# Performance work log

Measured on AMD Instinct MI355X. Metric: run time of the kernel, lower is better.

Reference implementation:

```python
import jax, jax.numpy as jnp
import numpy as np

N_HEAD = 8


def _forward(q, k, v, mask, gr_mask, adj, Wq, Wk, Wv, Wq2, Wk2, Wv2, Wfc,
             grW1, grb1, grW2, grb2, ln_g, ln_b):
    B, Lq, Eq, D = q.shape
    Lk, Ek = k.shape[1], k.shape[2]
    H = N_HEAD
    dk = Wq.shape[-1] // H
    dv = Wv.shape[-1] // H
    scale = dk ** 0.5
    # per-ensemble projections (i: q-ensemble, j: k-ensemble) -> [B,L,E,H,d]
    qp = jnp.einsum('blid,idf->blif', q, Wq).reshape(B, Lq, Eq, H, dk)
    qp2 = jnp.einsum('blid,idf->blif', q, Wq2).reshape(B, Lq, Eq, H, dk)
    kp = jnp.einsum('bljd,jdf->bljf', k, Wk).reshape(B, Lk, Ek, H, dk)
    kp2 = jnp.einsum('bljd,jdf->bljf', k, Wk2).reshape(B, Lk, Ek, H, dk)
    vp = jnp.einsum('bljd,jdf->bljf', v, Wv).reshape(B, Lk, Ek, H, dv)
    # (Wv2 projections are computed in the torch module but never used.)
    # scores for all (i, j, h) pairs at once: [B,Eq,H,Lq,Lk,Ek]
    s1 = jnp.einsum('bqihd,bkjhd->bihqkj', qp, kp) / scale
    s2 = jnp.einsum('bqihd,bkjhd->bihqkj', qp2, kp2) / scale
    at = jnp.tril(adj)[:, None, None, :, :, None]  # typed-edge gate
    scores = s1 * at + s2 * (1.0 - at)
    # gated graph-attention mask MLP, vectorized over (i,j,h)
    t = gr_mask.transpose(0, 2, 3, 1)  # [B,Lq,Lk,KG]
    h1 = jax.nn.relu(jnp.einsum('bqlg,ijhgm->ijhbqlm', t, grW1)
                     + grb1[:, :, :, None, None, None, :])
    agg = jnp.einsum('ijhbqlm,ijhm->ijhbql', h1, grW2) + grb2[:, :, :, None, None, None]
    agg = jnp.where(mask[None, None, None] == 1, agg, 0.0)  # zero where mask==0
    scores = scores + jnp.transpose(jax.nn.log_sigmoid(agg), (3, 0, 2, 4, 5, 1))
    scores = jnp.where(mask[:, None, None, :, :, None] == 0, -1e9, scores)
    # softmax jointly over (Lk, Ek), Ek fastest, matching the torch view
    attn = jax.nn.softmax(scores.reshape(B, Eq, H, Lq, Lk * Ek), axis=-1)
    attn = attn.reshape(B, Eq, H, Lq, Lk, Ek)
    pre = jnp.einsum('bihqke,bkehd->bqihd', attn, vp).reshape(B, Lq, Eq, H * dv)
    out = jnp.einsum('bqif,ifd->bqid', pre, Wfc) + q  # residual
    mu = out.mean(-1, keepdims=True)
    var = out.var(-1, keepdims=True)
    return (out - mu) / jnp.sqrt(var + 1e-6) * ln_g + ln_b


def setup_inputs() -> dict:
    ks = jax.random.split(jax.random.key(0), 16)
    B, L, Eq, Ek, D, KG = 4, 256, 2, 2, 512, 16
    H, dk, dv = N_HEAD, 64, 64
    s = 0.05
    return {
        'q': jax.random.normal(ks[0], (B, L, Eq, D)),
        'k': jax.random.normal(ks[1], (B, L, Ek, D)),
        'v': jax.random.normal(ks[2], (B, L, Ek, D)),
        'mask': jax.random.randint(ks[3], (B, L, L), 0, 2, dtype=jnp.int32),
        'gr_mask': jax.random.normal(ks[4], (B, KG, L, L)),
        'adj': jax.random.uniform(ks[5], (B, L, L)),
        'Wq': jax.random.normal(ks[6], (Eq, D, H * dk)) * s,
        'Wk': jax.random.normal(ks[7], (Ek, D, H * dk)) * s,
        'Wv': jax.random.normal(ks[8], (Ek, D, H * dv)) * s,
        'Wq2': jax.random.normal(ks[9], (Eq, D, H * dk)) * s,
        'Wk2': jax.random.normal(ks[10], (Ek, D, H * dk)) * s,
        'Wv2': jax.random.normal(ks[11], (Ek, D, H * dv)) * s,
        'Wfc': jax.random.normal(ks[12], (Eq, H * dv, D)) * s,
        'grW1': jax.random.normal(ks[13], (Eq, Ek, H, KG, KG)) * s,
        'grb1': jnp.zeros((Eq, Ek, H, KG)),
        'grW2': jax.random.normal(ks[14], (Eq, Ek, H, KG)) * s,
        'grb2': jnp.zeros((Eq, Ek, H)),
        'ln_g': jnp.ones((D,)),
        'ln_b': jnp.zeros((D,)),
    }


def reference(q, k, v, mask, gr_mask, adj, Wq, Wk, Wv, Wq2, Wk2, Wv2, Wfc,
              grW1, grb1, grW2, grb2, ln_g, ln_b):
    return _forward(q, k, v, mask, gr_mask, adj, Wq, Wk, Wv, Wq2, Wk2, Wv2, Wfc,
                    grW1, grb1, grW2, grb2, ln_g, ln_b)
```

## Files before the change

### kernel.cpp

```cpp
#include <hip/hip_runtime.h>


typedef short  s16x8 __attribute__((ext_vector_type(8)));
typedef float  f32x4 __attribute__((ext_vector_type(4)));

static __device__ __forceinline__ float4 ld4(const float* p) {
    return *reinterpret_cast<const float4*>(p);
}
static __device__ __forceinline__ ushort f2bf(float f) {
    unsigned u = __float_as_uint(f);
    return (ushort)((u + 0x7fffu + ((u >> 16) & 1u)) >> 16);
}
static __device__ __forceinline__ float bf2f(ushort u) {
    return __uint_as_float((unsigned)u << 16);
}

__global__ __launch_bounds__(256) void gemm_k(
    const float* __restrict__ qin, const float* __restrict__ kin, const float* __restrict__ vin,
    const float* __restrict__ Wq, const float* __restrict__ Wk, const float* __restrict__ Wv,
    const float* __restrict__ Wq2, const float* __restrict__ Wk2,
    const float* __restrict__ prebuf, const float* __restrict__ Wfc,
    ushort* __restrict__ qp, ushort* __restrict__ qp2, ushort* __restrict__ kp,
    ushort* __restrict__ kp2, ushort* __restrict__ vpT, float* __restrict__ fcb,
    int mm_base)
{
    __shared__ float As[64][17];
    __shared__ float Bs[16][64];

    const int mm = mm_base + (int)blockIdx.z;
    const float* A; const float* W; ushort* Du = nullptr; int ens; int mode;
    switch (mm) {
        case 0:  A=qin;    W=Wq;           Du=qp;   ens=0; mode=0; break;
        case 1:  A=qin;    W=Wq + 262144;  Du=qp;   ens=1; mode=0; break;
        case 2:  A=qin;    W=Wq2;          Du=qp2;  ens=0; mode=0; break;
        case 3:  A=qin;    W=Wq2 + 262144; Du=qp2;  ens=1; mode=0; break;
        case 4:  A=kin;    W=Wk;           Du=kp;   ens=0; mode=0; break;
        case 5:  A=kin;    W=Wk + 262144;  Du=kp;   ens=1; mode=0; break;
        case 6:  A=kin;    W=Wk2;          Du=kp2;  ens=0; mode=0; break;
        case 7:  A=kin;    W=Wk2 + 262144; Du=kp2;  ens=1; mode=0; break;
        case 8:  A=vin;    W=Wv;           Du=vpT;  ens=0; mode=1; break;
        case 9:  A=vin;    W=Wv + 262144;  Du=vpT;  ens=1; mode=1; break;
        case 10: A=prebuf; W=Wfc;                   ens=0; mode=2; break;
        default: A=prebuf; W=Wfc + 262144;          ens=1; mode=2; break;
    }

    const int tid = threadIdx.x;
    const int m0 = blockIdx.y * 64;
    const int n0 = blockIdx.x * 64;
    const int ty = tid >> 4, tx = tid & 15;
    const int ar = tid >> 2, ac = (tid & 3) * 4;
    const int br = tid >> 4, bc = (tid & 15) * 4;

    float acc[4][4] = {};

    for (int kt = 0; kt < 512; kt += 16) {
        float4 av = ld4(A + (size_t)(m0 + ar) * 1024 + ens * 512 + kt + ac);
        float4 bv = ld4(W + (size_t)(kt + br) * 512 + n0 + bc);
        __syncthreads();
        As[ar][ac + 0] = av.x; As[ar][ac + 1] = av.y;
        As[ar][ac + 2] = av.z; As[ar][ac + 3] = av.w;
        *reinterpret_cast<float4*>(&Bs[br][bc]) = bv;
        __syncthreads();
        #pragma unroll
        for (int kk = 0; kk < 16; ++kk) {
            float a0 = As[ty*4+0][kk];
            float a1 = As[ty*4+1][kk];
            float a2 = As[ty*4+2][kk];
            float a3 = As[ty*4+3][kk];
            float4 b4 = *reinterpret_cast<const float4*>(&Bs[kk][tx*4]);
            acc[0][0] += a0*b4.x; acc[0][1] += a0*b4.y; acc[0][2] += a0*b4.z; acc[0][3] += a0*b4.w;
            acc[1][0] += a1*b4.x; acc[1][1] += a1*b4.y; acc[1][2] += a1*b4.z; acc[1][3] += a1*b4.w;
            acc[2][0] += a2*b4.x; acc[2][1] += a2*b4.y; acc[2][2] += a2*b4.z; acc[2][3] += a2*b4.w;
            acc[3][0] += a3*b4.x; acc[3][1] += a3*b4.y; acc[3][2] += a3*b4.z; acc[3][3] += a3*b4.w;
        }
    }

    const int hh = n0 >> 6;
    if (mode == 0) {
        #pragma unroll
        for (int u = 0; u < 4; ++u) {
            const int m = m0 + ty * 4 + u;
            const int bb = m >> 8, l = m & 255;
            ushort4 o;
            o.x = f2bf(acc[u][0]); o.y = f2bf(acc[u][1]);
            o.z = f2bf(acc[u][2]); o.w = f2bf(acc[u][3]);
            *reinterpret_cast<ushort4*>(
                Du + ((size_t)((bb*2 + ens)*8 + hh) * 256 + l) * 64 + tx*4) = o;
        }
    } else if (mode == 1) {
        #pragma unroll
        for (int u = 0; u < 4; ++u) {
            const int m = m0 + ty * 4 + u;
            const int bb = m >> 8, l = m & 255;
            #pragma unroll
            for (int w = 0; w < 4; ++w) {
                const int d = tx*4 + w;
                Du[(size_t)(bb*8 + hh) * 32768 + (size_t)d * 512 + l*2 + ens] =
                    f2bf(acc[u][w]);
            }
        }
    } else {
        #pragma unroll
        for (int u = 0; u < 4; ++u) {
            const int m = m0 + ty * 4 + u;
            #pragma unroll
            for (int w = 0; w < 4; ++w)
                fcb[((size_t)m*2 + ens) * 512 + n0 + tx*4 + w] = acc[u][w];
        }
    }
}

__global__ __launch_bounds__(256) void mlp_mfma(
    const float* __restrict__ gr_mask, const int* __restrict__ mask,
    const float* __restrict__ grW1, const float* __restrict__ grb1,
    const float* __restrict__ grW2, const float* __restrict__ grb2,
    float* __restrict__ scores)
{
    __shared__ __align__(16) ushort ts[256][40];
    __shared__ __align__(16) ushort w1b[32][16][32];
    __shared__ __align__(16) float  b1s[32][16];
    __shared__ __align__(16) float  w2s[32][16];
    __shared__ float b2s[32];
    __shared__ ushort ls[256][33];

    const int tid = threadIdx.x;
    const int bq = blockIdx.x;
    const int b = bq >> 8, q = bq & 255;

    unsigned* w1w = (unsigned*)&w1b[0][0][0];
    #pragma unroll
    for (int it = 0; it < 32; ++it) w1w[tid + it*256] = 0;
    unsigned* tsw = (unsigned*)&ts[0][0];
    #pragma unroll
    for (int it = 0; it < 8; ++it) {
        int flat = tid + it*256;
        tsw[(flat >> 3) * 20 + 8 + (flat & 7)] = 0;
    }
    __syncthreads();

    #pragma unroll
    for (int g = 0; g < 16; ++g)
        ts[tid][g] = f2bf(gr_mask[(size_t)(b*16 + g) * 65536 + q*256 + tid]);
    #pragma unroll
    for (int it = 0; it < 32; ++it) {
        int flat = tid + it*256;
        int c = flat >> 8, m = (flat >> 4) & 15, g = flat & 15;
        w1b[c][m][g] = f2bf(grW1[c*256 + g*16 + m]);
    }
    #pragma unroll
    for (int it = 0; it < 2; ++it) {
        int flat = tid + it*256;
        b1s[flat >> 4][flat & 15] = grb1[flat];
        w2s[flat >> 4][flat & 15] = grW2[flat];
    }
    if (tid < 32) b2s[tid] = grb2[tid];
    __syncthreads();

    const int wv = tid >> 6, lane = tid & 63;
    const int lr = lane & 15, mg = lane >> 4;

    s16x8 tf[4];
    #pragma unroll
    for (int lt = 0; lt < 4; ++lt) {
        int l = (wv*4 + lt)*16 + lr;
        tf[lt] = *reinterpret_cast<const s16x8*>(&ts[l][mg*8]);
    }

    #pragma unroll 1
    for (int c = 0; c < 32; ++c) {
        s16x8 af  = *reinterpret_cast<const s16x8*>(&w1b[c][lr][mg*8]);
        f32x4 b1v = *reinterpret_cast<const f32x4*>(&b1s[c][mg*4]);
        f32x4 w2v = *reinterpret_cast<const f32x4*>(&w2s[c][mg*4]);
        const float b2v = b2s[c];

        f32x4 acc[4];
        #pragma unroll
        for (int lt = 0; lt < 4; ++lt)
            acc[lt] = __builtin_amdgcn_mfma_f32_16x16x32_bf16(af, tf[lt], b1v, 0, 0, 0);

        #pragma unroll
        for (int lt = 0; lt < 4; ++lt) {
            float s = fmaxf(acc[lt][0], 0.f) * w2v[0];
            s = fmaf(fmaxf(acc[lt][1], 0.f), w2v[1], s);
            s = fmaf(fmaxf(acc[lt][2], 0.f), w2v[2], s);
            s = fmaf(fmaxf(acc[lt][3], 0.f), w2v[3], s);
            s += __shfl_xor(s, 16);
            s += __shfl_xor(s, 32);
            if (lane < 16)
                ls[(wv*4 + lt)*16 + lane][c] = f2bf(s + b2v);
        }
    }
    __syncthreads();

    const int mv = mask[(size_t)(b*256 + q)*256 + tid];
    #pragma unroll 1
    for (int c2 = 0; c2 < 32; ++c2) {
        float agv = bf2f(ls[tid][c2]);
        if (mv == 0) agv = 0.f;
        float lsig = fminf(agv, 0.f) - log1pf(expf(-fabsf(agv)));
        int ii = c2 >> 4, jj = (c2 >> 3) & 1, hh = c2 & 7;
        scores[((size_t)((b*2 + ii)*8 + hh)*256 + q)*512 + (size_t)tid*2 + jj] = lsig;
    }
}

__global__ __launch_bounds__(256) void scores_mfma(
    const ushort* __restrict__ qp, const ushort* __restrict__ qp2,
    const ushort* __restrict__ kp, const ushort* __restrict__ kp2,
    const float* __restrict__ adj, const int* __restrict__ mask,
    float* __restrict__ scores)
{
    __shared__ __align__(16) ushort q1t[128*64];
    __shared__ __align__(16) ushort q2t[128*64];
    __shared__ __align__(16) ushort k1t[128*64];
    __shared__ __align__(16) ushort k2t[128*64];

    const int z = blockIdx.z;
    const int bih = z >> 1, j = z & 1;
    const int b = bih >> 4, h = bih & 7;
    const int bjh = (b*2 + j)*8 + h;
    const int q0 = blockIdx.x * 128, k0 = blockIdx.y * 128;
    const int tid = threadIdx.x;

    const ushort* gq1 = qp  + (size_t)bih * 16384 + q0 * 64;
    const ushort* gq2 = qp2 + (size_t)bih * 16384 + q0 * 64;
    const ushort* gk1 = kp  + (size_t)bjh * 16384 + k0 * 64;
    const ushort* gk2 = kp2 + (size_t)bjh * 16384 + k0 * 64;
    #pragma unroll
    for (int it = 0; it < 4; ++it) {
        int ch = tid + it * 256;
        int row = ch >> 3, c8 = ch & 7;
        int byte = row * 128 + c8 * 16; byte ^= (row & 7) << 4;
        *reinterpret_cast<uint4*>((char*)q1t + byte) = *reinterpret_cast<const uint4*>(gq1 + ch*8);
        *reinterpret_cast<uint4*>((char*)q2t + byte) = *reinterpret_cast<const uint4*>(gq2 + ch*8);
        *reinterpret_cast<uint4*>((char*)k1t + byte) = *reinterpret_cast<const uint4*>(gk1 + ch*8);
        *reinterpret_cast<uint4*>((char*)k2t + byte) = *reinterpret_cast<const uint4*>(gk2 + ch*8);
    }
    __syncthreads();

    const int wv = tid >> 6, lane = tid & 63;
    const int lr = lane & 15, kg = lane >> 4;

    #pragma unroll 1
    for (int qi = 0; qi < 2; ++qi) {
        const int qt = wv * 2 + qi;
        s16x8 a1[2], a2[2];
        #pragma unroll
        for (int ks = 0; ks < 2; ++ks) {
            int row = qt*16 + lr;
            int byte = row*128 + (ks*32 + kg*8)*2; byte ^= (row & 7) << 4;
            a1[ks] = *reinterpret_cast<const s16x8*>((const char*)q1t + byte);
            a2[ks] = *reinterpret_cast<const s16x8*>((const char*)q2t + byte);
        }
        #pragma unroll 1
        for (int kt = 0; kt < 8; ++kt) {
            f32x4 acc1 = {0.f, 0.f, 0.f, 0.f};
            f32x4 acc2 = {0.f, 0.f, 0.f, 0.f};
            #pragma unroll
            for (int ks = 0; ks < 2; ++ks) {
                int row = kt*16 + lr;
                int byte = row*128 + (ks*32 + kg*8)*2; byte ^= (row & 7) << 4;
                s16x8 b1 = *reinterpret_cast<const s16x8*>((const char*)k1t + byte);
                s16x8 b2 = *reinterpret_cast<const s16x8*>((const char*)k2t + byte);
                acc1 = __builtin_amdgcn_mfma_f32_16x16x32_bf16(a1[ks], b1, acc1, 0, 0, 0);
                acc2 = __builtin_amdgcn_mfma_f32_16x16x32_bf16(a2[ks], b2, acc2, 0, 0, 0);
            }
            const int kgl = k0 + kt*16 + lr;
            #pragma unroll
            for (int r = 0; r < 4; ++r) {
                const int qg = q0 + qt*16 + kg*4 + r;
                const size_t mi = (size_t)(b*256 + qg) * 256 + kgl;
                float gate = (qg >= kgl) ? adj[mi] : 0.f;
                float s = (acc1[r]*gate + acc2[r]*(1.f - gate)) * 0.125f;
                const size_t sidx = ((size_t)bih * 256 + qg) * 512 + (size_t)kgl * 2 + j;
                s += scores[sidx];
                if (mask[mi] == 0) s = -1e9f;
                scores[sidx] = s;
            }
        }
    }
}

__global__ __launch_bounds__(256) void softmax_k(float* __restrict__ scores,
                                                 ushort* __restrict__ attn_bf)
{
    const int row  = blockIdx.x * 4 + (threadIdx.x >> 6);
    const int lane = threadIdx.x & 63;
    float* p = scores + (size_t)row * 512 + lane * 8;
    float4 v0 = *reinterpret_cast<float4*>(p);
    float4 v1 = *reinterpret_cast<float4*>(p + 4);
    float v[8] = {v0.x, v0.y, v0.z, v0.w, v1.x, v1.y, v1.z, v1.w};

    float m = v[0];
    #pragma unroll
    for (int t = 1; t < 8; ++t) m = fmaxf(m, v[t]);
    #pragma unroll
    for (int off = 32; off > 0; off >>= 1) m = fmaxf(m, __shfl_xor(m, off));

    float s = 0.f;
    #pragma unroll
    for (int t = 0; t < 8; ++t) { v[t] = expf(v[t] - m); s += v[t]; }
    #pragma unroll
    for (int off = 32; off > 0; off >>= 1) s += __shfl_xor(s, off);

    const float inv = 1.f / s;
    #pragma unroll
    for (int t = 0; t < 8; ++t) v[t] *= inv;
    *reinterpret_cast<float4*>(p)     = make_float4(v[0], v[1], v[2], v[3]);
    *reinterpret_cast<float4*>(p + 4) = make_float4(v[4], v[5], v[6], v[7]);

    ushort* pb = attn_bf + (size_t)row * 512 + lane * 8;
    ushort4 lo, hi;
    lo.x = f2bf(v[0]); lo.y = f2bf(v[1]); lo.z = f2bf(v[2]); lo.w = f2bf(v[3]);
    hi.x = f2bf(v[4]); hi.y = f2bf(v[5]); hi.z = f2bf(v[6]); hi.w = f2bf(v[7]);
    *reinterpret_cast<ushort4*>(pb)     = lo;
    *reinterpret_cast<ushort4*>(pb + 4) = hi;
}

__global__ __launch_bounds__(256) void pv_mfma(
    const ushort* __restrict__ attn, const ushort* __restrict__ vpT,
    float* __restrict__ pre)
{
    __shared__ __align__(16) ushort at_t[64*128];
    __shared__ __align__(16) ushort v_t[64*128];

    const int bih = blockIdx.y;
    const int b = bih >> 4, i = (bih >> 3) & 1, h = bih & 7;
    const int q0 = blockIdx.x * 64;
    const int tid = threadIdx.x;
    const int wv = tid >> 6, lane = tid & 63;
    const int lr = lane & 15, kg = lane >> 4;

    const ushort* ga = attn + ((size_t)bih * 256 + q0) * 512;
    const ushort* gv = vpT + (size_t)(b*8 + h) * 32768;

    f32x4 acc[4];
    #pragma unroll
    for (int dt = 0; dt < 4; ++dt) acc[dt] = (f32x4){0.f, 0.f, 0.f, 0.f};

    #pragma unroll 1
    for (int kc = 0; kc < 4; ++kc) {
        __syncthreads();
        #pragma unroll
        for (int it = 0; it < 4; ++it) {
            int ch = tid + it * 256;
            int row = ch >> 4, c8 = ch & 15;
            int byte = row * 256 + c8 * 16; byte ^= (row & 7) << 4;
            *reinterpret_cast<uint4*>((char*)at_t + byte) =
                *reinterpret_cast<const uint4*>(ga + (size_t)row*512 + kc*128 + c8*8);
            *reinterpret_cast<uint4*>((char*)v_t + byte) =
                *reinterpret_cast<const uint4*>(gv + (size_t)row*512 + kc*128 + c8*8);
        }
        __syncthreads();
        #pragma unroll
        for (int ks = 0; ks < 4; ++ks) {
            int arow = wv*16 + lr;
            int abyte = arow*256 + (ks*32 + kg*8)*2; abyte ^= (arow & 7) << 4;
            s16x8 a = *reinterpret_cast<const s16x8*>((const char*)at_t + abyte);
            #pragma unroll
            for (int dt = 0; dt < 4; ++dt) {
                int vrow = dt*16 + lr;
                int vbyte = vrow*256 + (ks*32 + kg*8)*2; vbyte ^= (vrow & 7) << 4;
                s16x8 bv = *reinterpret_cast<const s16x8*>((const char*)v_t + vbyte);
                acc[dt] = __builtin_amdgcn_mfma_f32_16x16x32_bf16(a, bv, acc[dt], 0, 0, 0);
            }
        }
    }

    #pragma unroll
    for (int dt = 0; dt < 4; ++dt) {
        const int d = dt*16 + lr;
        #pragma unroll
        for (int r = 0; r < 4; ++r) {
            const int qg = q0 + wv*16 + kg*4 + r;
            pre[((size_t)(b*256 + qg)*2 + i) * 512 + h*64 + d] = acc[dt][r];
        }
    }
}

__global__ __launch_bounds__(256) void ln_k(
    const float* __restrict__ fcb, const float* __restrict__ qin,
    const float* __restrict__ lng, const float* __restrict__ lnb,
    float* __restrict__ out)
{
    __shared__ float red[8];
    const int row = blockIdx.x;
    const int tid = threadIdx.x;
    const float* fr = fcb + (size_t)row * 512;
    const float* qr = qin + (size_t)row * 512;
    float v0 = fr[tid]       + qr[tid];
    float v1 = fr[tid + 256] + qr[tid + 256];
    float s  = v0 + v1;
    float sq = v0*v0 + v1*v1;
    #pragma unroll
    for (int off = 32; off > 0; off >>= 1) {
        s  += __shfl_xor(s, off);
        sq += __shfl_xor(sq, off);
    }
    const int w = tid >> 6;
    if ((tid & 63) == 0) { red[w*2] = s; red[w*2 + 1] = sq; }
    __syncthreads();
    s  = red[0] + red[2] + red[4] + red[6];
    sq = red[1] + red[3] + red[5] + red[7];
    const float mu  = s * (1.f / 512.f);
    const float var = sq * (1.f / 512.f) - mu * mu;
    const float rs  = rsqrtf(var + 1e-6f);
    out[(size_t)row * 512 + tid]       = (v0 - mu) * rs * lng[tid]       + lnb[tid];
    out[(size_t)row * 512 + tid + 256] = (v1 - mu) * rs * lng[tid + 256] + lnb[tid + 256];
}

extern "C" void kernel_launch(void* const* d_in, const int* in_sizes, int n_in,
                              void* d_out, int out_size, void* d_ws, size_t ws_size,
                              hipStream_t stream) {
    (void)in_sizes; (void)n_in; (void)out_size; (void)ws_size;
    const float* qin    = (const float*)d_in[0];
    const float* kin    = (const float*)d_in[1];
    const float* vin    = (const float*)d_in[2];
    const int*   maskp  = (const int*)  d_in[3];
    const float* grm    = (const float*)d_in[4];
    const float* adj    = (const float*)d_in[5];
    const float* Wq     = (const float*)d_in[6];
    const float* Wk     = (const float*)d_in[7];
    const float* Wv     = (const float*)d_in[8];
    const float* Wq2    = (const float*)d_in[9];
    const float* Wk2    = (const float*)d_in[10];
    const float* Wfc    = (const float*)d_in[12];
    const float* grW1   = (const float*)d_in[13];
    const float* grb1   = (const float*)d_in[14];
    const float* grW2   = (const float*)d_in[15];
    const float* grb2   = (const float*)d_in[16];
    const float* lng    = (const float*)d_in[17];
    const float* lnb    = (const float*)d_in[18];
    float* out = (float*)d_out;

    char* w = (char*)d_ws;
    const size_t MB = 1048576;
    float*  scores  = (float*)(w);
    ushort* attn_bf = (ushort*)(w + 32*MB);
    float*  pre     = (float*) (w + 48*MB);
    ushort* qp_bf   = (ushort*)(w + 52*MB);
    ushort* qp2_bf  = (ushort*)(w + 54*MB);
    ushort* kp_bf   = (ushort*)(w + 56*MB);
    ushort* kp2_bf  = (ushort*)(w + 58*MB);
    ushort* vpT     = (ushort*)(w + 60*MB);
    float*  fcb     = (float*) (w + 52*MB);

    gemm_k<<<dim3(8, 16, 10), 256, 0, stream>>>(qin, kin, vin, Wq, Wk, Wv, Wq2, Wk2,
                                                pre, Wfc, qp_bf, qp2_bf, kp_bf, kp2_bf,
                                                vpT, fcb, 0);
    mlp_mfma<<<1024, 256, 0, stream>>>(grm, maskp, grW1, grb1, grW2, grb2, scores);
    scores_mfma<<<dim3(2, 2, 128), 256, 0, stream>>>(qp_bf, qp2_bf, kp_bf, kp2_bf,
                                                     adj, maskp, scores);
    softmax_k<<<4096, 256, 0, stream>>>(scores, attn_bf);
    pv_mfma<<<dim3(4, 64), 256, 0, stream>>>(attn_bf, vpT, pre);
    gemm_k<<<dim3(8, 16, 2), 256, 0, stream>>>(qin, kin, vin, Wq, Wk, Wv, Wq2, Wk2,
                                               pre, Wfc, qp_bf, qp2_bf, kp_bf, kp2_bf,
                                               vpT, fcb, 10);
    ln_k<<<2048, 256, 0, stream>>>(fcb, qin, lng, lnb, out);
}
```

Before: 373.5 us.

## Run projection and output GEMMs on bf16 MFMA with pre-transposed weights

Replaces the fp32 scalar-FMA tiled GEMM for the Q/K/V projections and the output FC with a bf16 MFMA kernel using 128x128 tiles and XOR-swizzled shared memory. A new conversion kernel transposes and converts each weight matrix to bf16 into workspace on every call, and activations are rounded to bf16 while being loaded. This is meant to cut the large fp32 ALU cost of the GEMMs, but it adds an extra weight pass plus launch and reduces precision on the projections and the final FC. The log-sigmoid in the mask MLP also switches to fast __expf/__logf intrinsics.

```diff
diff --git a/kernel.cpp b/kernel.cpp
--- a/kernel.cpp
+++ b/kernel.cpp
@@ -15,97 +15,160 @@
     return __uint_as_float((unsigned)u << 16);
 }
 
-__global__ __launch_bounds__(256) void gemm_k(
-    const float* __restrict__ qin, const float* __restrict__ kin, const float* __restrict__ vin,
-    const float* __restrict__ Wq, const float* __restrict__ Wk, const float* __restrict__ Wv,
-    const float* __restrict__ Wq2, const float* __restrict__ Wk2,
-    const float* __restrict__ prebuf, const float* __restrict__ Wfc,
+__global__ __launch_bounds__(256) void cvt_w(
+    const float* __restrict__ Wq, const float* __restrict__ Wq2,
+    const float* __restrict__ Wk, const float* __restrict__ Wk2,
+    const float* __restrict__ Wv, const float* __restrict__ Wfc,
+    ushort* __restrict__ WT, int base)
+{
+    __shared__ float tile[64][65];
+    const int mat = base + (int)blockIdx.z;
+    const float* src;
+    if (mat < 10) {
+        const float* sel;
+        switch (mat >> 1) {
+            case 0: sel = Wq;  break;
+            case 1: sel = Wq2; break;
+            case 2: sel = Wk;  break;
+            case 3: sel = Wk2; break;
+            default: sel = Wv; break;
+        }
+        src = sel + (mat & 1) * 262144;
+    } else {
+        src = Wfc + (mat - 10) * 262144;
+    }
+    ushort* dst = WT + (size_t)blockIdx.z * 262144;
+
+    const int tid = threadIdx.x;
+    const int n0 = blockIdx.x * 64, k0 = blockIdx.y * 64;
+    #pragma unroll
+    for (int it = 0; it < 4; ++it) {
+        int idx4 = tid + it * 256;
+        int kk = idx4 >> 4, c4 = (idx4 & 15) * 4;
+        float4 v = ld4(src + (size_t)(k0 + kk) * 512 + n0 + c4);
+        tile[kk][c4+0] = v.x; tile[kk][c4+1] = v.y;
+        tile[kk][c4+2] = v.z; tile[kk][c4+3] = v.w;
+    }
+    __syncthreads();
+    #pragma unroll
+    for (int it = 0; it < 4; ++it) {
+        int idx4 = tid + it * 256;
+        int n = idx4 >> 4, c4 = (idx4 & 15) * 4;
+        ushort4 o;
+        o.x = f2bf(tile[c4+0][n]); o.y = f2bf(tile[c4+1][n]);
+        o.z = f2bf(tile[c4+2][n]); o.w = f2bf(tile[c4+3][n]);
+        *reinterpret_cast<ushort4*>(dst + (size_t)(n0 + n) * 512 + k0 + c4) = o;
+    }
+}
+
+__global__ __launch_bounds__(256) void proj_mfma(
+    const float* __restrict__ qin, const float* __restrict__ kin,
+    const float* __restrict__ vin, const float* __restrict__ prebuf,
+    const ushort* __restrict__ WT,
     ushort* __restrict__ qp, ushort* __restrict__ qp2, ushort* __restrict__ kp,
     ushort* __restrict__ kp2, ushort* __restrict__ vpT, float* __restrict__ fcb,
     int mm_base)
 {
-    __shared__ float As[64][17];
-    __shared__ float Bs[16][64];
-
-    const int mm = mm_base + (int)blockIdx.z;
-    const float* A; const float* W; ushort* Du = nullptr; int ens; int mode;
+    __shared__ __align__(16) ushort At[128*64];
+    __shared__ __align__(16) ushort Wt[128*64];
+
+    const int z = blockIdx.z;
+    const int mm = mm_base + z;
+    const float* A; ushort* Du = nullptr; int ens; int mode;
     switch (mm) {
-        case 0:  A=qin;    W=Wq;           Du=qp;   ens=0; mode=0; break;
-        case 1:  A=qin;    W=Wq + 262144;  Du=qp;   ens=1; mode=0; break;
-        case 2:  A=qin;    W=Wq2;          Du=qp2;  ens=0; mode=0; break;
-        case 3:  A=qin;    W=Wq2 + 262144; Du=qp2;  ens=1; mode=0; break;
-        case 4:  A=kin;    W=Wk;           Du=kp;   ens=0; mode=0; break;
-        case 5:  A=kin;    W=Wk + 262144;  Du=kp;   ens=1; mode=0; break;
-        case 6:  A=kin;    W=Wk2;          Du=kp2;  ens=0; mode=0; break;
-        case 7:  A=kin;    W=Wk2 + 262144; Du=kp2;  ens=1; mode=0; break;
-        case 8:  A=vin;    W=Wv;           Du=vpT;  ens=0; mode=1; break;
-        case 9:  A=vin;    W=Wv + 262144;  Du=vpT;  ens=1; mode=1; break;
-        case 10: A=prebuf; W=Wfc;                   ens=0; mode=2; break;
-        default: A=prebuf; W=Wfc + 262144;          ens=1; mode=2; break;
-    }
+        case 0:  A=qin;    Du=qp;   ens=0; mode=0; break;
+        case 1:  A=qin;    Du=qp;   ens=1; mode=0; break;
+        case 2:  A=qin;    Du=qp2;  ens=0; mode=0; break;
+        case 3:  A=qin;    Du=qp2;  ens=1; mode=0; break;
+        case 4:  A=kin;    Du=kp;   ens=0; mode=0; break;
+        case 5:  A=kin;    Du=kp;   ens=1; mode=0; break;
+        case 6:  A=kin;    Du=kp2;  ens=0; mode=0; break;
+        case 7:  A=kin;    Du=kp2;  ens=1; mode=0; break;
+        case 8:  A=vin;    Du=vpT;  ens=0; mode=1; break;
+        case 9:  A=vin;    Du=vpT;  ens=1; mode=1; break;
+        case 10: A=prebuf;          ens=0; mode=2; break;
+        default: A=prebuf;          ens=1; mode=2; break;
+    }
+    const ushort* wt = WT + (size_t)z * 262144;
 
     const int tid = threadIdx.x;
-    const int m0 = blockIdx.y * 64;
-    const int n0 = blockIdx.x * 64;
-    const int ty = tid >> 4, tx = tid & 15;
-    const int ar = tid >> 2, ac = (tid & 3) * 4;
-    const int br = tid >> 4, bc = (tid & 15) * 4;
-
-    float acc[4][4] = {};
-
-    for (int kt = 0; kt < 512; kt += 16) {
-        float4 av = ld4(A + (size_t)(m0 + ar) * 1024 + ens * 512 + kt + ac);
-        float4 bv = ld4(W + (size_t)(kt + br) * 512 + n0 + bc);
+    const int m0 = blockIdx.y * 128;
+    const int n0 = blockIdx.x * 128;
+    const int wv = tid >> 6, lane = tid & 63;
+    const int lr = lane & 15, kg = lane >> 4;
+
+    f32x4 acc[2][8];
+    #pragma unroll
+    for (int qi = 0; qi < 2; ++qi)
+        #pragma unroll
+        for (int nt = 0; nt < 8; ++nt) acc[qi][nt] = (f32x4){0.f, 0.f, 0.f, 0.f};
+
+    #pragma unroll 1
+    for (int kc = 0; kc < 512; kc += 64) {
         __syncthreads();
-        As[ar][ac + 0] = av.x; As[ar][ac + 1] = av.y;
-        As[ar][ac + 2] = av.z; As[ar][ac + 3] = av.w;
-        *reinterpret_cast<float4*>(&Bs[br][bc]) = bv;
+        #pragma unroll
+        for (int it = 0; it < 8; ++it) {
+            int idx4 = tid + it * 256;
+            int m = idx4 >> 4, c4 = (idx4 & 15) * 4;
+            float4 v = ld4(A + (size_t)(m0 + m) * 1024 + ens * 512 + kc + c4);
+            ushort4 o;
+            o.x = f2bf(v.x); o.y = f2bf(v.y); o.z = f2bf(v.z); o.w = f2bf(v.w);
+            int byte = m * 128 + c4 * 2; byte ^= (m & 7) << 4;
+            *reinterpret_cast<ushort4*>((char*)At + byte) = o;
+        }
+        #pragma unroll
+        for (int it = 0; it < 4; ++it) {
+            int idx8 = tid + it * 256;
+            int n = idx8 >> 3, c8 = idx8 & 7;
+            int byte = n * 128 + c8 * 16; byte ^= (n & 7) << 4;
+            *reinterpret_cast<uint4*>((char*)Wt + byte) =
+                *reinterpret_cast<const uint4*>(wt + (size_t)(n0 + n) * 512 + kc + c8 * 8);
+        }
         __syncthreads();
-        #pragma unroll
-        for (int kk = 0; kk < 16; ++kk) {
-            float a0 = As[ty*4+0][kk];
-            float a1 = As[ty*4+1][kk];
-            float a2 = As[ty*4+2][kk];
-            float a3 = As[ty*4+3][kk];
-            float4 b4 = *reinterpret_cast<const float4*>(&Bs[kk][tx*4]);
-            acc[0][0] += a0*b4.x; acc[0][1] += a0*b4.y; acc[0][2] += a0*b4.z; acc[0][3] += a0*b4.w;
-            acc[1][0] += a1*b4.x; acc[1][1] += a1*b4.y; acc[1][2] += a1*b4.z; acc[1][3] += a1*b4.w;
-            acc[2][0] += a2*b4.x; acc[2][1] += a2*b4.y; acc[2][2] += a2*b4.z; acc[2][3] += a2*b4.w;
-            acc[3][0] += a3*b4.x; acc[3][1] += a3*b4.y; acc[3][2] += a3*b4.z; acc[3][3] += a3*b4.w;
-        }
-    }
-
-    const int hh = n0 >> 6;
-    if (mode == 0) {
-        #pragma unroll
-        for (int u = 0; u < 4; ++u) {
-            const int m = m0 + ty * 4 + u;
-            const int bb = m >> 8, l = m & 255;
-            ushort4 o;
-            o.x = f2bf(acc[u][0]); o.y = f2bf(acc[u][1]);
-            o.z = f2bf(acc[u][2]); o.w = f2bf(acc[u][3]);
-            *reinterpret_cast<ushort4*>(
-                Du + ((size_t)((bb*2 + ens)*8 + hh) * 256 + l) * 64 + tx*4) = o;
-        }
-    } else if (mode == 1) {
-        #pragma unroll
-        for (int u = 0; u < 4; ++u) {
-            const int m = m0 + ty * 4 + u;
-            const int bb = m >> 8, l = m & 255;
+
+        s16x8 af[2][2];
+        #pragma unroll
+        for (int qi = 0; qi < 2; ++qi)
             #pragma unroll
-            for (int w = 0; w < 4; ++w) {
-                const int d = tx*4 + w;
-                Du[(size_t)(bb*8 + hh) * 32768 + (size_t)d * 512 + l*2 + ens] =
-                    f2bf(acc[u][w]);
+            for (int ks = 0; ks < 2; ++ks) {
+                int row = (wv*2 + qi)*16 + lr;
+                int byte = row*128 + (ks*32 + kg*8)*2; byte ^= (row & 7) << 4;
+                af[qi][ks] = *reinterpret_cast<const s16x8*>((const char*)At + byte);
             }
-        }
-    } else {
-        #pragma unroll
-        for (int u = 0; u < 4; ++u) {
-            const int m = m0 + ty * 4 + u;
+        #pragma unroll
+        for (int nt = 0; nt < 8; ++nt) {
+            int row = nt*16 + lr;
+            int byte0 = row*128 + (kg*8)*2;      byte0 ^= (row & 7) << 4;
+            int byte1 = row*128 + (32 + kg*8)*2; byte1 ^= (row & 7) << 4;
+            s16x8 b0 = *reinterpret_cast<const s16x8*>((const char*)Wt + byte0);
+            s16x8 b1 = *reinterpret_cast<const s16x8*>((const char*)Wt + byte1);
             #pragma unroll
-            for (int w = 0; w < 4; ++w)
-                fcb[((size_t)m*2 + ens) * 512 + n0 + tx*4 + w] = acc[u][w];
+            for (int qi = 0; qi < 2; ++qi) {
+                acc[qi][nt] = __builtin_amdgcn_mfma_f32_16x16x32_bf16(af[qi][0], b0, acc[qi][nt], 0, 0, 0);
+                acc[qi][nt] = __builtin_amdgcn_mfma_f32_16x16x32_bf16(af[qi][1], b1, acc[qi][nt], 0, 0, 0);
+            }
+        }
+    }
+
+    #pragma unroll
+    for (int qi = 0; qi < 2; ++qi) {
+        #pragma unroll
+        for (int nt = 0; nt < 8; ++nt) {
+            const int n = n0 + nt*16 + lr;
+            const int hh = n >> 6, d = n & 63;
+            #pragma unroll
+            for (int r = 0; r < 4; ++r) {
+                const int m = m0 + (wv*2 + qi)*16 + kg*4 + r;
+                const int bb = m >> 8, l = m & 255;
+                const float val = acc[qi][nt][r];
+                if (mode == 0) {
+                    Du[((size_t)((bb*2 + ens)*8 + hh) * 256 + l) * 64 + d] = f2bf(val);
+                } else if (mode == 1) {
+                    Du[(size_t)(bb*8 + hh) * 32768 + (size_t)d * 512 + l*2 + ens] = f2bf(val);
+                } else {
+                    fcb[((size_t)m*2 + ens) * 512 + n] = val;
+                }
+            }
         }
     }
 }
@@ -197,7 +260,7 @@
     for (int c2 = 0; c2 < 32; ++c2) {
         float agv = bf2f(ls[tid][c2]);
         if (mv == 0) agv = 0.f;
-        float lsig = fminf(agv, 0.f) - log1pf(expf(-fabsf(agv)));
+        float lsig = fminf(agv, 0.f) - __logf(1.f + __expf(-fabsf(agv)));
         int ii = c2 >> 4, jj = (c2 >> 3) & 1, hh = c2 & 7;
         scores[((size_t)((b*2 + ii)*8 + hh)*256 + q)*512 + (size_t)tid*2 + jj] = lsig;
     }
@@ -436,6 +499,7 @@
     const size_t MB = 1048576;
     float*  scores  = (float*)(w);
     ushort* attn_bf = (ushort*)(w + 32*MB);
+    ushort* WT      = (ushort*)(w + 32*MB);
     float*  pre     = (float*) (w + 48*MB);
     ushort* qp_bf   = (ushort*)(w + 52*MB);
     ushort* qp2_bf  = (ushort*)(w + 54*MB);
@@ -444,16 +508,18 @@
     ushort* vpT     = (ushort*)(w + 60*MB);
     float*  fcb     = (float*) (w + 52*MB);
 
-    gemm_k<<<dim3(8, 16, 10), 256, 0, stream>>>(qin, kin, vin, Wq, Wk, Wv, Wq2, Wk2,
-                                                pre, Wfc, qp_bf, qp2_bf, kp_bf, kp2_bf,
-                                                vpT, fcb, 0);
+    cvt_w<<<dim3(8, 8, 10), 256, 0, stream>>>(Wq, Wq2, Wk, Wk2, Wv, Wfc, WT, 0);
+    proj_mfma<<<dim3(4, 8, 10), 256, 0, stream>>>(qin, kin, vin, pre, WT,
+                                                  qp_bf, qp2_bf, kp_bf, kp2_bf,
+                                                  vpT, fcb, 0);
     mlp_mfma<<<1024, 256, 0, stream>>>(grm, maskp, grW1, grb1, grW2, grb2, scores);
     scores_mfma<<<dim3(2, 2, 128), 256, 0, stream>>>(qp_bf, qp2_bf, kp_bf, kp2_bf,
                                                      adj, maskp, scores);
     softmax_k<<<4096, 256, 0, stream>>>(scores, attn_bf);
     pv_mfma<<<dim3(4, 64), 256, 0, stream>>>(attn_bf, vpT, pre);
-    gemm_k<<<dim3(8, 16, 2), 256, 0, stream>>>(qin, kin, vin, Wq, Wk, Wv, Wq2, Wk2,
-                                               pre, Wfc, qp_bf, qp2_bf, kp_bf, kp2_bf,
-                                               vpT, fcb, 10);
+    cvt_w<<<dim3(8, 8, 2), 256, 0, stream>>>(Wq, Wq2, Wk, Wk2, Wv, Wfc, WT, 10);
+    proj_mfma<<<dim3(4, 8, 2), 256, 0, stream>>>(qin, kin, vin, pre, WT,
+                                                 qp_bf, qp2_bf, kp_bf, kp2_bf,
+                                                 vpT, fcb, 10);
     ln_k<<<2048, 256, 0, stream>>>(fcb, qin, lng, lnb, out);
 }
```

After: 305.8 us. -18.1%, faster.
